# Optimization experiments

Hardware: AMD Instinct MI355X
Metric: run time of the kernel (lower is better)

Reference implementation:

```python
import jax, jax.numpy as jnp
import numpy as np

B, S, D, H = 2, 2048, 1024, 16
DH = D // H  # head dim = 64


def _split_heads(x):
    # [B,S,D] -> [B,H,S,DH]
    return x.reshape(B, S, H, DH).transpose(0, 2, 1, 3)


def setup_inputs() -> dict:
    key = jax.random.key(0)
    ks = jax.random.split(key, 14)
    sc = 1.0 / np.sqrt(D)
    p = {"hidden_states": jax.random.normal(ks[0], (B, S, D), jnp.float32)}
    names = ["Wq", "Wk1", "Wk2", "Wv1", "Wv2", "Wd"]
    for i, n in enumerate(names):
        p[n] = jax.random.normal(ks[1 + 2 * i], (D, D), jnp.float32) * sc
        p["b" + n[1:]] = jax.random.normal(ks[2 + 2 * i], (D,), jnp.float32) * 0.02
    return p


def reference(hidden_states, Wq, bq, Wk1, bk1, Wk2, bk2, Wv1, bv1, Wv2, bv2, Wd, bd):
    q = _split_heads(hidden_states @ Wq + bq)
    k1 = _split_heads(hidden_states @ Wk1 + bk1)
    k2 = _split_heads(hidden_states @ Wk2 + bk2)
    v1 = _split_heads(hidden_states @ Wv1 + bv1)
    v2 = _split_heads(hidden_states @ Wv2 + bv2)

    scores = jnp.einsum("bhqd,bhkd->bhqk", q, k1) / np.sqrt(DH)
    causal = jnp.tril(jnp.ones((S, S), dtype=bool))  # True = keep
    scores = jnp.where(causal, scores, -jnp.inf)
    probs = jax.nn.softmax(scores, axis=-1)

    ctx = jnp.einsum("bhqk,bhkd->bhqd", probs, v1)          # [B,H,S,DH]
    ctx = jnp.einsum("bhqd,bhkd->bhqk", ctx, k2)            # [B,H,S,S]
    ctx = jnp.einsum("bhqk,bhkd->bhqd", ctx, v2)            # [B,H,S,DH]

    ctx = ctx.transpose(0, 2, 1, 3).reshape(B, S, D)
    return ctx @ Wd + bd
```

## Files before the change

### kernel.cpp

```cpp
#include <hip/hip_runtime.h>
#include <hip/hip_bf16.h>

typedef __bf16 bf16x8 __attribute__((ext_vector_type(8)));
typedef float f32x4 __attribute__((ext_vector_type(4)));
using bf16 = __hip_bfloat16;

#define SEQ 2048
#define DM 1024
#define NH 16
#define DH 64
#define NBH 32
#define MR 4096

#define WAITBAR(N) asm volatile("s_waitcnt vmcnt(" #N ")\n\ts_barrier" ::: "memory")

static __device__ __forceinline__ void async_cp16(const void* gsrc, void* ldsdst) {
  __builtin_amdgcn_global_load_lds((__attribute__((address_space(1))) void*)gsrc,
                                   (__attribute__((address_space(3))) void*)ldsdst, 16, 0, 0);
}

static __device__ __forceinline__ unsigned short f2bfu(float f) {
  bf16 h = __float2bfloat16(f);
  unsigned short u; __builtin_memcpy(&u, &h, 2); return u;
}
static __device__ __forceinline__ unsigned int pack_bf2(float lo, float hi) {
  return (unsigned int)f2bfu(lo) | ((unsigned int)f2bfu(hi) << 16);
}

__global__ __launch_bounds__(256) void cast_x(const float* __restrict__ X, bf16* __restrict__ Xb) {
  long g = ((long)blockIdx.x * 256 + threadIdx.x) * 8;
  float4 a = *(const float4*)(X + g);
  float4 b = *(const float4*)(X + g + 4);
  unsigned short u[8];
  u[0]=f2bfu(a.x); u[1]=f2bfu(a.y); u[2]=f2bfu(a.z); u[3]=f2bfu(a.w);
  u[4]=f2bfu(b.x); u[5]=f2bfu(b.y); u[6]=f2bfu(b.z); u[7]=f2bfu(b.w);
  uint4 o; __builtin_memcpy(&o, u, 16);
  *(uint4*)(Xb + g) = o;
}

struct WPtrs { const float* w[6]; };

__global__ __launch_bounds__(256) void transpose_cast_w(WPtrs wp, bf16* __restrict__ WtAll) {
  const int z = blockIdx.z;
  const float* W = wp.w[z];
  bf16* Wt = WtAll + (long)z * DM * DM;
  __shared__ float Ts[32][33];
  int n0 = blockIdx.x * 32, k0 = blockIdx.y * 32;
  int tx = threadIdx.x, ty = threadIdx.y;
#pragma unroll
  for (int it = 0; it < 4; ++it)
    Ts[ty + 8*it][tx] = W[(long)(k0 + ty + 8*it) * DM + n0 + tx];
  __syncthreads();
#pragma unroll
  for (int it = 0; it < 4; ++it)
    Wt[(long)(n0 + ty + 8*it) * DM + k0 + tx] = __float2bfloat16(Ts[tx][ty + 8*it]);
}

struct ProjArgs {
  const float* bias[5];
  bf16* out[5];
};

__global__ __launch_bounds__(256, 2) void gemm_proj(const bf16* __restrict__ A,
                                                    const bf16* __restrict__ WtAll, ProjArgs p) {
  __shared__ alignas(16) bf16 SM[36864];
  bf16* As = SM;
  bf16* Bs = SM + 12288;
  const int tid = threadIdx.x;
  const int bid = blockIdx.x;
  const int mt = bid & 31, nt = bid >> 5;
  const int m0 = mt * 128;
  const int z = nt >> 2;
  const int n0z = (nt & 3) * 256;
  const bf16* Bt = WtAll + (long)z * DM * DM + (long)n0z * DM;

  const int wave = tid >> 6, lane = tid & 63, l15 = lane & 15, l4 = lane >> 4;
  const int wm = wave >> 1, wn = wave & 1;

  const int prow = tid >> 2;
  const int cc = (tid & 3) ^ ((prow >> 1) & 3);
  const bf16* sA0 = A  + (long)(m0 + prow) * DM + cc * 8;
  const bf16* sA1 = sA0 + 64L * DM;
  const bf16* sB0 = Bt + (long)prow * DM + cc * 8;
  const bf16* sB1 = sB0 + 64L * DM;
  const bf16* sB2 = sB0 + 128L * DM;
  const bf16* sB3 = sB0 + 192L * DM;
  char* dA = (char*)As + wave * 1024;
  char* dB = (char*)Bs + wave * 1024;

#define PSTAGE(KT_, BUF_) do {                                  \
    int ko_ = (KT_) * 32;                                       \
    async_cp16(sA0 + ko_, dA + (BUF_) * 8192);                  \
    async_cp16(sA1 + ko_, dA + (BUF_) * 8192 + 4096);           \
    async_cp16(sB0 + ko_, dB + (BUF_) * 16384);                 \
    async_cp16(sB1 + ko_, dB + (BUF_) * 16384 + 4096);          \
    async_cp16(sB2 + ko_, dB + (BUF_) * 16384 + 8192);          \
    async_cp16(sB3 + ko_, dB + (BUF_) * 16384 + 12288);         \
  } while (0)

  const int slot8 = (l4 ^ ((l15 >> 1) & 3)) * 8;
  const int arow = wm * 64 + l15;
  const int brow = wn * 128 + l15;
  f32x4 acc[4][8] = {};

#define PCOMPUTE(BUF_) do {                                                        \
    const bf16* ab_ = As + (BUF_) * 4096;                                          \
    const bf16* bb_ = Bs + (BUF_) * 8192;                                          \
    bf16x8 af_[4], bq_[8];                                                         \
    _Pragma("unroll")                                                              \
    for (int i = 0; i < 4; ++i) af_[i] = *(const bf16x8*)(ab_ + (arow + i * 16) * 32 + slot8); \
    _Pragma("unroll")                                                              \
    for (int j = 0; j < 8; ++j) bq_[j] = *(const bf16x8*)(bb_ + (brow + j * 16) * 32 + slot8); \
    _Pragma("unroll")                                                              \
    for (int i = 0; i < 4; ++i)                                                    \
      _Pragma("unroll")                                                            \
      for (int j = 0; j < 8; ++j)                                                  \
        acc[i][j] = __builtin_amdgcn_mfma_f32_16x16x32_bf16(af_[i], bq_[j], acc[i][j], 0, 0, 0); \
  } while (0)

  PSTAGE(0, 0);
  PSTAGE(1, 1);
  int buf = 0;
#pragma unroll 1
  for (int k = 0; k < 31; ++k) {
    WAITBAR(6);
    if (k < 30) {
      int nb = buf + 2; if (nb > 2) nb -= 3;
      PSTAGE(k + 2, nb);
    }
    PCOMPUTE(buf);
    ++buf; if (buf > 2) buf = 0;
  }
  WAITBAR(0);
  PCOMPUTE(buf);
#undef PSTAGE
#undef PCOMPUTE

  const float* bias = p.bias[z];
  bf16* out = p.out[z];
  float bv[8];
#pragma unroll
  for (int j = 0; j < 8; ++j) bv[j] = bias[n0z + wn * 128 + j * 16 + l15];

  if (z < 2) {
    const float scale = (z == 0) ? 0.125f * 1.44269504f : 1.0f;
#pragma unroll
    for (int i = 0; i < 4; ++i)
#pragma unroll
      for (int j = 0; j < 8; ++j)
#pragma unroll
        for (int r = 0; r < 4; ++r) {
          int m = m0 + wm * 64 + i * 16 + l4 * 4 + r;
          int n = n0z + wn * 128 + j * 16 + l15;
          int b = m >> 11, s = m & 2047, hh = n >> 6, d = n & 63;
          out[((long)((b * NH + hh) * SEQ + s)) * DH + d] =
              __float2bfloat16((acc[i][j][r] + bv[j]) * scale);
        }
  } else {
    __syncthreads();
    bf16* Os = SM;
#pragma unroll
    for (int i = 0; i < 4; ++i)
#pragma unroll
      for (int j = 0; j < 8; ++j)
#pragma unroll
        for (int r = 0; r < 4; ++r) {
          int nl = wn * 128 + j * 16 + l15;
          int ml = wm * 64 + i * 16 + l4 * 4 + r;
          Os[nl * 136 + ml] = __float2bfloat16(acc[i][j][r] + bv[j]);
        }
    __syncthreads();
    {
      int nl = tid;
      int ng = n0z + nl;
      int hh = ng >> 6, d = ng & 63;
      int b = m0 >> 11, s0 = m0 & 2047;
      bf16* op = out + ((long)((b * NH + hh) * DH + d)) * SEQ + s0;
#pragma unroll
      for (int u = 0; u < 16; ++u)
        *(bf16x8*)(op + u * 8) = *(const bf16x8*)(Os + nl * 136 + u * 8);
    }
  }
}

static __device__ __forceinline__ void gemm_core128(
    const bf16* __restrict__ A, const bf16* __restrict__ Bt,
    bf16* As, bf16* Bs, f32x4 (&acc)[4][4], int m0, int tid)
{
  const int wave = tid >> 6, lane = tid & 63, l15 = lane & 15, l4 = lane >> 4;
  const int wm = wave >> 1, wn = wave & 1;
  const int r0 = tid >> 2;
  const int c0 = (tid & 3) ^ ((r0 >> 1) & 3);
  const bf16* srcA0 = A + (long)(m0 + r0) * DM + c0 * 8;
  const bf16* srcA1 = A + (long)(m0 + r0 + 64) * DM + c0 * 8;
  const bf16* srcB0 = Bt + (long)r0 * DM + c0 * 8;
  const bf16* srcB1 = Bt + (long)(r0 + 64) * DM + c0 * 8;
  char* dstA = (char*)As + wave * 1024;
  char* dstB = (char*)Bs + wave * 1024;

#define STAGE(KT_, BUF_) do {                                   \
    int ko_ = (KT_) * 32;                                       \
    int bo_ = (BUF_) * 8192;                                    \
    async_cp16(srcA0 + ko_, dstA + bo_);                        \
    async_cp16(srcA1 + ko_, dstA + bo_ + 4096);                 \
    async_cp16(srcB0 + ko_, dstB + bo_);                        \
    async_cp16(srcB1 + ko_, dstB + bo_ + 4096);                 \
  } while (0)

  const int slot8 = (l4 ^ ((l15 >> 1) & 3)) * 8;
  const int arow = wm * 64 + l15;
  const int brow = wn * 64 + l15;

#define COMPUTE(BUF_) do {                                                         \
    const bf16* ab_ = As + (BUF_) * 4096;                                          \
    const bf16* bb_ = Bs + (BUF_) * 4096;                                          \
    bf16x8 af_[4], bq_[4];                                                         \
    _Pragma("unroll")                                                              \
    for (int i = 0; i < 4; ++i) af_[i] = *(const bf16x8*)(ab_ + (arow + i * 16) * 32 + slot8); \
    _Pragma("unroll")                                                              \
    for (int j = 0; j < 4; ++j) bq_[j] = *(const bf16x8*)(bb_ + (brow + j * 16) * 32 + slot8); \
    _Pragma("unroll")                                                              \
    for (int i = 0; i < 4; ++i)                                                    \
      _Pragma("unroll")                                                            \
      for (int j = 0; j < 4; ++j)                                                  \
        acc[i][j] = __builtin_amdgcn_mfma_f32_16x16x32_bf16(af_[i], bq_[j], acc[i][j], 0, 0, 0); \
  } while (0)

  STAGE(0, 0);
  STAGE(1, 1);
  int buf = 0;
#pragma unroll 1
  for (int k = 0; k < 31; ++k) {
    WAITBAR(4);
    if (k < 30) {
      int nb = buf + 2; if (nb > 2) nb -= 3;
      STAGE(k + 2, nb);
    }
    COMPUTE(buf);
    ++buf; if (buf > 2) buf = 0;
  }
  WAITBAR(0);
  COMPUTE(buf);
#undef STAGE
#undef COMPUTE
}

__global__ __launch_bounds__(256, 3) void gemm_out(const bf16* __restrict__ A, const bf16* __restrict__ Bt,
                                                   const float* __restrict__ bias, float* __restrict__ out) {
  __shared__ alignas(16) bf16 As[3 * 128 * 32];
  __shared__ alignas(16) bf16 Bs[3 * 128 * 32];
  const int tid = threadIdx.x;
  const int bid = blockIdx.x;
  const int nt = bid & 7, mt = bid >> 3;
  const int m0 = mt * 128, n0 = nt * 128;
  f32x4 acc[4][4] = {};
  gemm_core128(A, Bt + (long)n0 * DM, As, Bs, acc, m0, tid);
  const int wave = tid >> 6, lane = tid & 63, l15 = lane & 15, l4 = lane >> 4;
  const int wm = wave >> 1, wn = wave & 1;
  float bv[4];
#pragma unroll
  for (int j = 0; j < 4; ++j) bv[j] = bias[n0 + wn * 64 + j * 16 + l15];
#pragma unroll
  for (int i = 0; i < 4; ++i)
#pragma unroll
    for (int j = 0; j < 4; ++j)
#pragma unroll
      for (int r = 0; r < 4; ++r) {
        int m = m0 + wm * 64 + i * 16 + l4 * 4 + r;
        int n = n0 + wn * 64 + j * 16 + l15;
        out[(long)m * DM + n] = acc[i][j][r] + bv[j];
      }
}

__global__ __launch_bounds__(256) void m_kernel(
    const bf16* __restrict__ k2t, const bf16* __restrict__ v2t, float* __restrict__ Mbuf)
{
  const int scx = blockIdx.x;
  const int bh = blockIdx.y;
  const int tid = threadIdx.x, wave = tid >> 6, lane = tid & 63, l15 = lane & 15, l4 = lane >> 4;
  const bf16* kp = k2t + (long)bh * DH * SEQ;
  const bf16* vp = v2t + (long)bh * DH * SEQ;
  __shared__ alignas(16) bf16 K2s[64 * 32];
  __shared__ alignas(16) bf16 V2s[64 * 32];
  f32x4 acc[4] = {};
  const int s0 = scx * 256;
  for (int kk = 0; kk < 256; kk += 32) {
    __syncthreads();
    {
      int c = tid, r = c >> 2, pp = c & 3;
      async_cp16(kp + (long)r * SEQ + s0 + kk + pp * 8, K2s + wave * 64 * 8);
      async_cp16(vp + (long)r * SEQ + s0 + kk + pp * 8, V2s + wave * 64 * 8);
    }
    __syncthreads();
    int arow = 16 * wave + l15;
    bf16x8 a = *(const bf16x8*)(K2s + arow * 32 + l4 * 8);
#pragma unroll
    for (int nb = 0; nb < 4; ++nb) {
      int col = nb * 16 + l15;
      bf16x8 b = *(const bf16x8*)(V2s + col * 32 + l4 * 8);
      acc[nb] = __builtin_amdgcn_mfma_f32_16x16x32_bf16(a, b, acc[nb], 0, 0, 0);
    }
  }
  float* Mp = Mbuf + (long)bh * 4096;
#pragma unroll
  for (int nb = 0; nb < 4; ++nb)
#pragma unroll
    for (int r = 0; r < 4; ++r) {
      int row = 16 * wave + l4 * 4 + r;
      int col = nb * 16 + l15;
      atomicAdd(Mp + row * 64 + col, acc[nb][r]);
    }
}

static __device__ __forceinline__ void redist(const unsigned int (&pk)[4][2], bf16x8 (&pb)[2],
                                              int l4, int l15) {
#pragma unroll
  for (int h = 0; h < 2; ++h) {
    unsigned int w4[4];
#pragma unroll
    for (int w = 0; w < 4; ++w) {
      int src = l15 + 16 * (2 * (l4 & 1) + (w >> 1));
      unsigned int va = (unsigned int)__shfl((int)pk[2 * h][w & 1], src);
      unsigned int vb = (unsigned int)__shfl((int)pk[2 * h + 1][w & 1], src);
      w4[w] = (l4 & 2) ? vb : va;
    }
    __builtin_memcpy(&pb[h], w4, 16);
  }
}

__global__ __launch_bounds__(256) void attn_fused(
    const bf16* __restrict__ q,
    const bf16* __restrict__ k1,
    const bf16* __restrict__ v1t,
    const float* __restrict__ Mbuf,
    bf16* __restrict__ ctx2)
{
  const int qpair = blockIdx.x;
  const int bh = blockIdx.y;
  const int bb = bh >> 4, hh = bh & 15;
  const int tid = threadIdx.x, wave = tid >> 6, lane = tid & 63;
  const int l15 = lane & 15, l4 = lane >> 4;
  const bf16* qp = q   + (long)bh * SEQ * DH;
  const bf16* kp = k1  + (long)bh * SEQ * DH;
  const bf16* vp = v1t + (long)bh * DH * SEQ;
  const float* Mp = Mbuf + (long)bh * 4096;

  __shared__ alignas(16) bf16 Ks[2][128 * 64];
  __shared__ alignas(16) bf16 Vs[2][64 * 128];

  bf16x8 mf[4][2];
#pragma unroll
  for (int db = 0; db < 4; ++db)
#pragma unroll
    for (int h = 0; h < 2; ++h) {
      bf16x8 t;
#pragma unroll
      for (int j = 0; j < 8; ++j)
        t[j] = (__bf16)Mp[(32 * h + 8 * l4 + j) * 64 + 16 * db + l15];
      mf[db][h] = t;
    }

#define STAGE_KV(JJ, BUF) do {                                                     \
    int kv0_ = 128 * (JJ);                                                         \
    int cK_ = (tid & 7) ^ ((tid >> 3) & 7);                                        \
    int cV_ = (tid & 15) ^ ((tid >> 4) & 15);                                      \
    _Pragma("unroll")                                                              \
    for (int p_ = 0; p_ < 4; ++p_) {                                               \
      int rK_ = (tid >> 3) + 32 * p_;                                              \
      async_cp16(kp + (long)(kv0_ + rK_) * DH + cK_ * 8,                           \
                 (char*)Ks[BUF] + p_ * 4096 + wave * 1024);                        \
      int rV_ = (tid >> 4) + 16 * p_;                                              \
      async_cp16(vp + (long)rV_ * SEQ + kv0_ + cV_ * 8,                            \
                 (char*)Vs[BUF] + p_ * 4096 + wave * 1024);                        \
    }                                                                              \
  } while (0)

#pragma unroll 1
  for (int half = 0; half < 2; ++half) {
    const int tq = (half == 0) ? (31 - qpair) : qpair;
    const int Q0 = 64 * tq;
    const int qg = Q0 + 16 * wave + l15;
    const int jm = tq >> 1;

    __syncthreads();
    STAGE_KV(0, 0);

    bf16x8 aq[2];
#pragma unroll
    for (int h = 0; h < 2; ++h)
      aq[h] = *(const bf16x8*)(qp + (long)qg * DH + 32 * h + 8 * l4);

    float m_run = -__builtin_inff(), l_run = 0.f;
    f32x4 acc_o[4] = {};

    __syncthreads();

#pragma unroll 1
    for (int j = 0; j <= jm; ++j) {
      const int cur = j & 1;
      if (j < jm) STAGE_KV(j + 1, cur ^ 1);

      f32x4 sc[8] = {};
#pragma unroll
      for (int nb = 0; nb < 8; ++nb) {
        const bf16* krow = Ks[cur] + (16 * nb + l15) * 64;
#pragma unroll
        for (int h = 0; h < 2; ++h) {
          bf16x8 kf = *(const bf16x8*)(krow + (((4 * h + l4) ^ (l15 & 7)) * 8));
          sc[nb] = __builtin_amdgcn_mfma_f32_16x16x32_bf16(kf, aq[h], sc[nb], 0, 0, 0);
        }
      }

      if (j == jm) {
        const int kv0 = 128 * j;
#pragma unroll
        for (int nb = 0; nb < 8; ++nb)
#pragma unroll
          for (int r = 0; r < 4; ++r)
            if (kv0 + 16 * nb + 4 * l4 + r > qg) sc[nb][r] = -__builtin_inff();
      }

      float tmax = -__builtin_inff();
#pragma unroll
      for (int nb = 0; nb < 8; ++nb)
#pragma unroll
        for (int r = 0; r < 4; ++r) tmax = fmaxf(tmax, sc[nb][r]);
      tmax = fmaxf(tmax, __shfl_xor(tmax, 16));
      tmax = fmaxf(tmax, __shfl_xor(tmax, 32));
      float mnew = fmaxf(m_run, tmax);
      float sf = __builtin_amdgcn_exp2f(m_run - mnew);
      m_run = mnew;

      float ssum = 0.f;
      unsigned int pkA[4][2], pkB[4][2];
#pragma unroll
      for (int nb = 0; nb < 4; ++nb)
#pragma unroll
        for (int pr = 0; pr < 2; ++pr) {
          float p0 = __builtin_amdgcn_exp2f(sc[nb][2 * pr]     - mnew);
          float p1 = __builtin_amdgcn_exp2f(sc[nb][2 * pr + 1] - mnew);
          ssum += p0 + p1;
          pkA[nb][pr] = pack_bf2(p0, p1);
        }
#pragma unroll
      for (int nb = 0; nb < 4; ++nb)
#pragma unroll
        for (int pr = 0; pr < 2; ++pr) {
          float p0 = __builtin_amdgcn_exp2f(sc[nb + 4][2 * pr]     - mnew);
          float p1 = __builtin_amdgcn_exp2f(sc[nb + 4][2 * pr + 1] - mnew);
          ssum += p0 + p1;
          pkB[nb][pr] = pack_bf2(p0, p1);
        }
      ssum += __shfl_xor(ssum, 16);
      ssum += __shfl_xor(ssum, 32);
      l_run = l_run * sf + ssum;
#pragma unroll
      for (int db = 0; db < 4; ++db)
#pragma unroll
        for (int r = 0; r < 4; ++r) acc_o[db][r] *= sf;

      bf16x8 pbA[2], pbB[2];
      redist(pkA, pbA, l4, l15);
      redist(pkB, pbB, l4, l15);
#pragma unroll
      for (int db = 0; db < 4; ++db) {
        const bf16* vrow = Vs[cur] + (16 * db + l15) * 128;
#pragma unroll
        for (int hs = 0; hs < 2; ++hs) {
          bf16x8 vf = *(const bf16x8*)(vrow + (((4 * hs + l4) ^ l15) * 8));
          acc_o[db] = __builtin_amdgcn_mfma_f32_16x16x32_bf16(vf, pbA[hs], acc_o[db], 0, 0, 0);
        }
#pragma unroll
        for (int hs = 0; hs < 2; ++hs) {
          bf16x8 vf = *(const bf16x8*)(vrow + (((4 * (hs + 2) + l4) ^ l15) * 8));
          acc_o[db] = __builtin_amdgcn_mfma_f32_16x16x32_bf16(vf, pbB[hs], acc_o[db], 0, 0, 0);
        }
      }
      __syncthreads();
    }

    float invl = __builtin_amdgcn_rcpf(l_run);
    unsigned int ck[4][2];
#pragma unroll
    for (int db = 0; db < 4; ++db)
#pragma unroll
      for (int pr = 0; pr < 2; ++pr)
        ck[db][pr] = pack_bf2(acc_o[db][2 * pr] * invl, acc_o[db][2 * pr + 1] * invl);
    bf16x8 cb[2];
    redist(ck, cb, l4, l15);
    f32x4 o2[4] = {};
#pragma unroll
    for (int db = 0; db < 4; ++db)
#pragma unroll
      for (int h = 0; h < 2; ++h)
        o2[db] = __builtin_amdgcn_mfma_f32_16x16x32_bf16(mf[db][h], cb[h], o2[db], 0, 0, 0);

    bf16* Os = (bf16*)Ks;
#pragma unroll
    for (int db = 0; db < 4; ++db)
#pragma unroll
      for (int r = 0; r < 4; ++r)
        Os[(16 * wave + l15) * 72 + 16 * db + 4 * l4 + r] = __float2bfloat16(o2[db][r]);
    __syncthreads();
    {
      int rr = tid >> 2, cc2 = tid & 3;
      long obase = ((long)(bb * SEQ + Q0 + rr)) * DM + hh * DH + cc2 * 16;
      *(bf16x8*)(ctx2 + obase)     = *(const bf16x8*)(Os + rr * 72 + cc2 * 16);
      *(bf16x8*)(ctx2 + obase + 8) = *(const bf16x8*)(Os + rr * 72 + cc2 * 16 + 8);
    }
  }
#undef STAGE_KV
}

extern "C" void kernel_launch(void* const* d_in, const int* in_sizes, int n_in,
                              void* d_out, int out_size, void* d_ws, size_t ws_size,
                              hipStream_t stream) {
  (void)in_sizes; (void)n_in; (void)out_size; (void)ws_size;
  const float* X = (const float*)d_in[0];
  const float* W[6]    = {(const float*)d_in[1], (const float*)d_in[3], (const float*)d_in[5],
                          (const float*)d_in[7], (const float*)d_in[9], (const float*)d_in[11]};
  const float* bias[6] = {(const float*)d_in[2], (const float*)d_in[4], (const float*)d_in[6],
                          (const float*)d_in[8], (const float*)d_in[10], (const float*)d_in[12]};

  char* ws = (char*)d_ws;
  bf16* Xb  = (bf16*)(ws);
  bf16* Wt  = (bf16*)(ws + (8L  << 20));
  bf16* qB  = (bf16*)(ws + (20L << 20));
  bf16* k1B = (bf16*)(ws + (28L << 20));
  bf16* k2t = (bf16*)(ws + (36L << 20));
  bf16* v1t = (bf16*)(ws + (44L << 20));
  bf16* v2t = (bf16*)(ws + (52L << 20));
  float* Mb = (float*)(ws + (60L << 20));
  bf16* c2  = Xb;

  cast_x<<<2048, 256, 0, stream>>>(X, Xb);

  WPtrs wp; for (int z = 0; z < 6; ++z) wp.w[z] = W[z];
  transpose_cast_w<<<dim3(32, 32, 6), dim3(32, 8), 0, stream>>>(wp, Wt);

  ProjArgs pa;
  for (int z = 0; z < 5; ++z) pa.bias[z] = bias[z];
  pa.out[0] = qB; pa.out[1] = k1B; pa.out[2] = k2t; pa.out[3] = v1t; pa.out[4] = v2t;
  gemm_proj<<<640, 256, 0, stream>>>(Xb, Wt, pa);

  hipMemsetAsync(Mb, 0, (size_t)NBH * 4096 * 4, stream);
  m_kernel<<<dim3(8, 32), 256, 0, stream>>>(k2t, v2t, Mb);

  attn_fused<<<dim3(16, 32), 256, 0, stream>>>(qB, k1B, v1t, Mb, c2);

  gemm_out<<<256, 256, 0, stream>>>(c2, Wt + 5L * DM * DM, bias[5], (float*)d_out);
}
```

Baseline: 161.0 us.

## Shrink projection GEMM LDS to double buffering for three blocks per CU

The projection GEMM drops from a triple-buffered to a double-buffered LDS pipeline, shrinking shared memory so launch bounds can target three blocks per CU instead of two. The transposed-output epilogue is split into two passes so its staging fits in the smaller LDS buffer. Higher occupancy is meant to hide memory latency better. In exchange, prefetch depth falls to one stage, each iteration waits for all outstanding loads, and the tighter register budget may cause spills with the 4x8 accumulator tile.

```diff
diff --git a/kernel.cpp b/kernel.cpp
--- a/kernel.cpp
+++ b/kernel.cpp
@@ -61,11 +61,11 @@
   bf16* out[5];
 };
 
-__global__ __launch_bounds__(256, 2) void gemm_proj(const bf16* __restrict__ A,
+__global__ __launch_bounds__(256, 3) void gemm_proj(const bf16* __restrict__ A,
                                                     const bf16* __restrict__ WtAll, ProjArgs p) {
-  __shared__ alignas(16) bf16 SM[36864];
+  __shared__ alignas(16) bf16 SM[24576];
   bf16* As = SM;
-  bf16* Bs = SM + 12288;
+  bf16* Bs = SM + 8192;
   const int tid = threadIdx.x;
   const int bid = blockIdx.x;
   const int mt = bid & 31, nt = bid >> 5;
@@ -119,20 +119,14 @@
   } while (0)
 
   PSTAGE(0, 0);
-  PSTAGE(1, 1);
   int buf = 0;
 #pragma unroll 1
-  for (int k = 0; k < 31; ++k) {
-    WAITBAR(6);
-    if (k < 30) {
-      int nb = buf + 2; if (nb > 2) nb -= 3;
-      PSTAGE(k + 2, nb);
-    }
+  for (int k = 0; k < 32; ++k) {
+    WAITBAR(0);
+    if (k < 31) PSTAGE(k + 1, buf ^ 1);
     PCOMPUTE(buf);
-    ++buf; if (buf > 2) buf = 0;
+    buf ^= 1;
   }
-  WAITBAR(0);
-  PCOMPUTE(buf);
 #undef PSTAGE
 #undef PCOMPUTE
 
@@ -157,28 +151,33 @@
               __float2bfloat16((acc[i][j][r] + bv[j]) * scale);
         }
   } else {
-    __syncthreads();
+    const int b = m0 >> 11, s0 = m0 & 2047;
     bf16* Os = SM;
-#pragma unroll
-    for (int i = 0; i < 4; ++i)
-#pragma unroll
-      for (int j = 0; j < 8; ++j)
-#pragma unroll
-        for (int r = 0; r < 4; ++r) {
-          int nl = wn * 128 + j * 16 + l15;
-          int ml = wm * 64 + i * 16 + l4 * 4 + r;
-          Os[nl * 136 + ml] = __float2bfloat16(acc[i][j][r] + bv[j]);
-        }
-    __syncthreads();
-    {
-      int nl = tid;
-      int ng = n0z + nl;
-      int hh = ng >> 6, d = ng & 63;
-      int b = m0 >> 11, s0 = m0 & 2047;
-      bf16* op = out + ((long)((b * NH + hh) * DH + d)) * SEQ + s0;
-#pragma unroll
-      for (int u = 0; u < 16; ++u)
-        *(bf16x8*)(op + u * 8) = *(const bf16x8*)(Os + nl * 136 + u * 8);
+#pragma unroll 1
+    for (int pass = 0; pass < 2; ++pass) {
+      __syncthreads();
+#pragma unroll
+      for (int i = 0; i < 4; ++i)
+#pragma unroll
+        for (int jj = 0; jj < 4; ++jj) {
+          int j = 4 * pass + jj;
+#pragma unroll
+          for (int r = 0; r < 4; ++r) {
+            int br = wn * 64 + jj * 16 + l15;
+            int ml = wm * 64 + i * 16 + l4 * 4 + r;
+            Os[br * 136 + ml] = __float2bfloat16(acc[i][j][r] + bv[j]);
+          }
+        }
+      __syncthreads();
+      {
+        int br = tid & 127, hseg = tid >> 7;
+        int ng = n0z + (br >> 6) * 128 + 64 * pass + (br & 63);
+        int hh2 = ng >> 6, d = ng & 63;
+        bf16* op = out + ((long)((b * NH + hh2) * DH + d)) * SEQ + s0 + hseg * 64;
+#pragma unroll
+        for (int u = 0; u < 8; ++u)
+          *(bf16x8*)(op + u * 8) = *(const bf16x8*)(Os + br * 136 + hseg * 64 + u * 8);
+      }
     }
   }
 }
```

After: 201.6 us. 25.2% more time.
